# Performance work log

Hardware: AMD Instinct MI355X
Metric: run time of the kernel (lower is better)

## Reference

```python
import jax, jax.numpy as jnp
import numpy as np

INPUT_SIZE = 1024
HIDDEN_SIZE = 1024
BATCH = 4096


def setup_inputs() -> dict:
    key = jax.random.key(0)
    ks = jax.random.split(key, 20)
    k = 1.0 / HIDDEN_SIZE
    bound = float(np.sqrt(k))

    def u(kk, shape):
        return jax.random.uniform(kk, shape, jnp.float32, -bound, bound)

    inp = {
        "x": jax.random.normal(ks[0], (BATCH, INPUT_SIZE), jnp.float32),
        "h0": jax.random.normal(ks[1], (BATCH, HIDDEN_SIZE), jnp.float32),
        "c0": jax.random.normal(ks[2], (BATCH, HIDDEN_SIZE), jnp.float32),
        "W_ii": u(ks[3], (INPUT_SIZE, HIDDEN_SIZE)), "b_ii": u(ks[4], (HIDDEN_SIZE,)),
        "W_if": u(ks[5], (INPUT_SIZE, HIDDEN_SIZE)), "b_if": u(ks[6], (HIDDEN_SIZE,)),
        "W_ig": u(ks[7], (INPUT_SIZE, HIDDEN_SIZE)), "b_ig": u(ks[8], (HIDDEN_SIZE,)),
        "W_io": u(ks[9], (INPUT_SIZE, HIDDEN_SIZE)), "b_io": u(ks[10], (HIDDEN_SIZE,)),
        "W_hi": u(ks[11], (HIDDEN_SIZE, HIDDEN_SIZE)), "b_hi": u(ks[12], (HIDDEN_SIZE,)),
        "W_hf": u(ks[13], (HIDDEN_SIZE, HIDDEN_SIZE)), "b_hf": u(ks[14], (HIDDEN_SIZE,)),
        "W_hg": u(ks[15], (HIDDEN_SIZE, HIDDEN_SIZE)), "b_hg": u(ks[16], (HIDDEN_SIZE,)),
        "W_ho": u(ks[17], (HIDDEN_SIZE, HIDDEN_SIZE)), "b_ho": u(ks[18], (HIDDEN_SIZE,)),
    }
    return inp


def reference(x, h0, c0,
              W_ii, b_ii, W_if, b_if, W_ig, b_ig, W_io, b_io,
              W_hi, b_hi, W_hf, b_hf, W_hg, b_hg, W_ho, b_ho):
    # Fuse the 4 input-side and 4 hidden-side GEMMs into two wide GEMMs,
    # then a single fused gate computation — same math as the original.
    Wi = jnp.concatenate([W_ii, W_if, W_ig, W_io], axis=1)  # [In, 4H]
    Wh = jnp.concatenate([W_hi, W_hf, W_hg, W_ho], axis=1)  # [H, 4H]
    b = jnp.concatenate([b_ii + b_hi, b_if + b_hf, b_ig + b_hg, b_io + b_ho])
    gates = x @ Wi + h0 @ Wh + b  # [B, 4H]
    zi, zf, zg, zo = jnp.split(gates, 4, axis=1)
    i = jax.nn.sigmoid(zi)
    f = jax.nn.sigmoid(zf)
    g = jnp.tanh(zg)
    o = jax.nn.sigmoid(zo)
    c1 = f * c0 + i * g
    h1 = o * c1
    return h1, c1
```

## Files before the change

kernel.cpp:

```cpp
#include <hip/hip_runtime.h>

typedef unsigned short u16;
typedef unsigned int u32;
typedef __attribute__((ext_vector_type(8))) short short8;
typedef __attribute__((ext_vector_type(4))) float f32x4;

__device__ __forceinline__ u16 f2b(float f) {
  u32 u = __builtin_bit_cast(u32, f);
  u32 r = (u + 0x7FFFu + ((u >> 16) & 1u)) >> 16;
  return (u16)r;
}

__device__ __forceinline__ void gl_lds16(const void* g, void* l) {
  __builtin_amdgcn_global_load_lds(
      (const __attribute__((address_space(1))) u32*)g,
      (__attribute__((address_space(3))) u32*)l, 16, 0, 0);
}

struct Ptrs8 { const float* p[8]; };

__global__ __launch_bounds__(256) void wt_pack(Ptrs8 w, u16* __restrict__ Wt) {
  __shared__ float lds[64 * 64];
  const int tid = threadIdx.x;
  const int bid = blockIdx.x;
  const int mat = bid >> 8;
  const int g = mat & 3, h = mat >> 2;
  const int tile = bid & 255;
  const int kt = tile >> 4, nt = tile & 15;
  const float* __restrict__ src = w.p[mat];

#pragma unroll
  for (int i = 0; i < 4; ++i) {
    int c = tid + i * 256;
    int k = c >> 4, n4 = (c & 15) * 4;
    gl_lds16(src + (size_t)(kt * 64 + k) * 1024 + nt * 64 + n4, &lds[c * 4]);
  }
  asm volatile("s_waitcnt vmcnt(0)");
  __syncthreads();

#pragma unroll
  for (int i = 0; i < 2; ++i) {
    int c = tid + i * 256;
    int n = c & 63, kb = (c >> 6) * 8;
    short8 v;
#pragma unroll
    for (int j = 0; j < 8; ++j) v[j] = (short)f2b(lds[(kb + j) * 64 + n]);
    size_t off = (size_t)(g * 1024 + nt * 64 + n) * 2048 + h * 1024 + kt * 64 + kb;
    *reinterpret_cast<short8*>(Wt + off) = v;
  }
}

__global__ __launch_bounds__(256) void xh_pack(const float* __restrict__ x,
                                               const float* __restrict__ h0,
                                               u16* __restrict__ Ap) {
  int t = blockIdx.x * 256 + threadIdx.x;
  int m = t >> 8, kc = t & 255;
  const float* src = (kc < 128) ? (x + (size_t)m * 1024 + kc * 8)
                                : (h0 + (size_t)m * 1024 + (kc - 128) * 8);
  float4 a = *reinterpret_cast<const float4*>(src);
  float4 b = *reinterpret_cast<const float4*>(src + 4);
  short8 v;
  v[0] = (short)f2b(a.x); v[1] = (short)f2b(a.y);
  v[2] = (short)f2b(a.z); v[3] = (short)f2b(a.w);
  v[4] = (short)f2b(b.x); v[5] = (short)f2b(b.y);
  v[6] = (short)f2b(b.z); v[7] = (short)f2b(b.w);
  *reinterpret_cast<short8*>(Ap + (size_t)m * 2048 + kc * 8) = v;
}

__global__ void bias_pack(Ptrs8 b, float* __restrict__ bias) {
  int i = blockIdx.x * 1024 + threadIdx.x;
  int g = i >> 10, n = i & 1023;
  bias[i] = b.p[g][n] + b.p[4 + g][n];
}

#define LD8(base, off) (*reinterpret_cast<const short8*>((base) + (off)))
#define MFMA_(a, b, c) __builtin_amdgcn_mfma_f32_16x16x32_bf16(a, b, c, 0, 0, 0)
#define PIN asm volatile("" ::: "memory")
#define SB0 __builtin_amdgcn_sched_barrier(0)
#define BARR __builtin_amdgcn_s_barrier()
#define PRIO1 __builtin_amdgcn_s_setprio(1);
#define PRIO0 __builtin_amdgcn_s_setprio(0);

#define READ_A(DST, BASE)                                   \
  _Pragma("unroll")                                         \
  for (int mi = 0; mi < 4; ++mi) {                          \
    DST[mi][0] = LD8(Ab, arow + (BASE + mi) * 1024 + c0k);  \
    DST[mi][1] = LD8(Ab, arow + (BASE + mi) * 1024 + c1k);  \
  }
#define READ_B(DST, GB)                                     \
  _Pragma("unroll")                                         \
  for (int g = 0; g < 2; ++g) {                             \
    DST[g][0] = LD8(Bb, bbase + (GB + g) * 4096 + c0k);     \
    DST[g][1] = LD8(Bb, bbase + (GB + g) * 4096 + c1k);     \
  }
#define MFMA_QUAD(AF, BF, MO, GO)                                              \
  _Pragma("unroll")                                                            \
  for (int mi = 0; mi < 4; ++mi)                                               \
    _Pragma("unroll")                                                          \
    for (int g = 0; g < 2; ++g) {                                              \
      acc[MO + mi][GO + g] = MFMA_(AF[mi][0], BF[g][0], acc[MO + mi][GO + g]); \
      acc[MO + mi][GO + g] = MFMA_(AF[mi][1], BF[g][1], acc[MO + mi][GO + g]); \
    }

#define TILE4(BUF, T, ST, TAILW)                                             \
  {                                                                          \
    const u16* Ab = &As[BUF][0];                                             \
    const u16* Bb = &Bs[BUF][0];                                             \
    short8 af03[4][2], af47[4][2], bf01[2][2], bf23[2][2];                   \
                                               \
    READ_A(af03, 0) READ_B(bf01, 0) PIN;                                     \
    BARR;                                                                    \
    asm volatile("s_waitcnt lgkmcnt(0)"); SB0;                               \
    PRIO1 MFMA_QUAD(af03, bf01, 0, 0) PRIO0                                  \
    BARR; PIN;                                                               \
                                 \
    READ_B(bf23, 2) PIN;                                                     \
    if (ST) { stageA(BUF, (T) + 2, 0); stageB(BUF, (T) + 2, 0); }            \
    PIN;                                                                     \
    BARR;                                                                    \
    asm volatile("s_waitcnt lgkmcnt(0)"); SB0;                               \
    PRIO1 MFMA_QUAD(af03, bf23, 0, 2) PRIO0                                  \
    BARR; PIN;                                                               \
                                     \
    READ_A(af47, 4) PIN;                                                     \
    if (ST) { stageB(BUF, (T) + 2, 1); }                                     \
    PIN;                                                                     \
    BARR;                                                                    \
    asm volatile("s_waitcnt lgkmcnt(0)"); SB0;                               \
    PRIO1 MFMA_QUAD(af47, bf01, 4, 0) PRIO0                                  \
    BARR; PIN;                                                               \
                                       \
    if (ST) { stageA(BUF, (T) + 2, 1); }                                     \
    PIN;                                                                     \
    PRIO1 MFMA_QUAD(af47, bf23, 4, 2) PRIO0                                  \
    if ((TAILW) == 8) asm volatile("s_waitcnt vmcnt(8)" ::: "memory");       \
    else if ((TAILW) == 0) asm volatile("s_waitcnt vmcnt(0)" ::: "memory");  \
    BARR; PIN;                                                               \
  }

__global__ __launch_bounds__(512, 2) void lstm_fused(
    const u16* __restrict__ Ap, const float* __restrict__ c0,
    const u16* __restrict__ Wt, const float* __restrict__ bias,
    float* __restrict__ out) {
  __shared__ u16 As[2][256 * 64];
  __shared__ u16 Bs[2][256 * 64];

  const int tid = threadIdx.x;
  const int lane = tid & 63;
  const int wid = tid >> 6;
  const int wr = wid >> 2;
  const int wc = wid & 3;
  const int fl = lane & 15;
  const int hi = lane >> 4;
  const int lo7 = fl & 7;

  const int bid0 = blockIdx.x;
  const int sbid = (bid0 & 7) * 32 + (bid0 >> 3);
  const int m0 = (sbid >> 4) * 256;
  const int n0 = (sbid & 15) * 64;

  int aoff[4], boff[4];
#pragma unroll
  for (int i = 0; i < 4; ++i) {
    const int L = tid + i * 512;
    const int r = L >> 3, cL = L & 7;
    const int cg = cL ^ (r & 7);
    aoff[i] = (m0 + r) * 2048 + cg * 8;
    const int ge = r >> 6, wce = (r >> 4) & 3, ue = r & 15;
    boff[i] = (ge * 1024 + n0 + wce * 16 + ue) * 2048 + cg * 8;
  }

  auto stageA = [&](int buf, int t, int h) {
    const int k0 = t * 64;
    gl_lds16(Ap + aoff[h] + k0, &As[buf][(tid + h * 512) * 8]);
    gl_lds16(Ap + aoff[h + 2] + k0, &As[buf][(tid + (h + 2) * 512) * 8]);
  };
  auto stageB = [&](int buf, int t, int h) {
    const int k0 = t * 64;
    gl_lds16(Wt + boff[2 * h] + k0, &Bs[buf][(tid + (2 * h) * 512) * 8]);
    gl_lds16(Wt + boff[2 * h + 1] + k0, &Bs[buf][(tid + (2 * h + 1) * 512) * 8]);
  };

  const int c0k = (hi ^ lo7) * 8;
  const int c1k = ((4 + hi) ^ lo7) * 8;
  const int arow = (wr * 128 + fl) * 64;
  const int bbase = (wc * 16 + fl) * 64;

  f32x4 acc[8][4] = {};

  stageA(0, 0, 0); stageB(0, 0, 0); stageB(0, 0, 1); stageA(0, 0, 1);
  stageA(1, 1, 0); stageB(1, 1, 0); stageB(1, 1, 1); stageA(1, 1, 1);
  asm volatile("s_waitcnt vmcnt(8)" ::: "memory");
  BARR; PIN;

  for (int i = 0; i < 15; ++i) {
    TILE4(0, 2 * i, 1, 8)
    TILE4(1, 2 * i + 1, 1, 8)
  }
  TILE4(0, 30, 0, 0)
  TILE4(1, 31, 0, -1)

  const int col = n0 + wc * 16 + fl;
  float bv[4];
#pragma unroll
  for (int g = 0; g < 4; ++g) bv[g] = bias[g * 1024 + col];

#pragma unroll
  for (int mi = 0; mi < 8; ++mi) {
#pragma unroll
    for (int r = 0; r < 4; ++r) {
      const int row = m0 + wr * 128 + mi * 16 + hi * 4 + r;
      const float zi = acc[mi][0][r] + bv[0];
      const float zf = acc[mi][1][r] + bv[1];
      const float zg = acc[mi][2][r] + bv[2];
      const float zo = acc[mi][3][r] + bv[3];
      const float ig = 1.f / (1.f + __expf(-zi));
      const float fg = 1.f / (1.f + __expf(-zf));
      const float gg = 1.f - 2.f / (__expf(2.f * zg) + 1.f);
      const float og = 1.f / (1.f + __expf(-zo));
      const float c0v = c0[(size_t)row * 1024 + col];
      const float c1 = fg * c0v + ig * gg;
      const float h1 = og * c1;
      out[(size_t)row * 1024 + col] = h1;
      out[(size_t)4194304 + (size_t)row * 1024 + col] = c1;
    }
  }
}

extern "C" void kernel_launch(void* const* d_in, const int* in_sizes, int n_in,
                              void* d_out, int out_size, void* d_ws, size_t ws_size,
                              hipStream_t stream) {
  const float* x  = (const float*)d_in[0];
  const float* h0 = (const float*)d_in[1];
  const float* c0 = (const float*)d_in[2];
  Ptrs8 w, b;
  for (int i = 0; i < 4; ++i) {
    w.p[i]     = (const float*)d_in[3 + 2 * i];
    b.p[i]     = (const float*)d_in[4 + 2 * i];
    w.p[4 + i] = (const float*)d_in[11 + 2 * i];
    b.p[4 + i] = (const float*)d_in[12 + 2 * i];
  }
  u16* Wt = (u16*)d_ws;
  u16* Ap = (u16*)((char*)d_ws + (size_t)4096 * 2048 * 2);
  float* bias = (float*)((char*)d_ws + (size_t)2 * 4096 * 2048 * 2);
  float* out = (float*)d_out;

  wt_pack<<<2048, 256, 0, stream>>>(w, Wt);
  xh_pack<<<4096, 256, 0, stream>>>(x, h0, Ap);
  bias_pack<<<4, 1024, 0, stream>>>(b, bias);
  lstm_fused<<<256, 512, 0, stream>>>(Ap, c0, Wt, bias, out);
}
```

Measured before the change: 92.72 us.

## Merge pack kernels into one launch and restructure GEMM LDS pipeline

Merges the three preprocessing kernels (weight transpose and pack, activation pack, bias sum) into one prepack kernel that picks its role from the block index, which removes two launch gaps. The main LSTM GEMM loop now prefetches the next tile into the other buffer while computing the current one, instead of staging tile t+2 into the current buffer. It also trims the per-quarter barriers from two to one and uses finer vmcnt waits. The risk is a shorter prefetch distance, which may expose more global load latency, plus more delicate barrier and wait correctness.

```diff
diff --git a/kernel.cpp b/kernel.cpp
--- a/kernel.cpp
+++ b/kernel.cpp
@@ -19,67 +19,67 @@
 
 struct Ptrs8 { const float* p[8]; };
 
-__global__ __launch_bounds__(256) void wt_pack(Ptrs8 w, u16* __restrict__ Wt) {
+__global__ __launch_bounds__(256) void prepack(Ptrs8 w, Ptrs8 b,
+                                               const float* __restrict__ x,
+                                               const float* __restrict__ h0,
+                                               u16* __restrict__ Wt,
+                                               u16* __restrict__ Ap,
+                                               float* __restrict__ bias) {
   __shared__ float lds[64 * 64];
   const int tid = threadIdx.x;
   const int bid = blockIdx.x;
-  const int mat = bid >> 8;
-  const int g = mat & 3, h = mat >> 2;
-  const int tile = bid & 255;
-  const int kt = tile >> 4, nt = tile & 15;
-  const float* __restrict__ src = w.p[mat];
-
-#pragma unroll
-  for (int i = 0; i < 4; ++i) {
-    int c = tid + i * 256;
-    int k = c >> 4, n4 = (c & 15) * 4;
-    gl_lds16(src + (size_t)(kt * 64 + k) * 1024 + nt * 64 + n4, &lds[c * 4]);
-  }
-  asm volatile("s_waitcnt vmcnt(0)");
-  __syncthreads();
-
-#pragma unroll
-  for (int i = 0; i < 2; ++i) {
-    int c = tid + i * 256;
-    int n = c & 63, kb = (c >> 6) * 8;
+
+  if (bid < 2048) {
+    const int mat = bid >> 8;
+    const int g = mat & 3, h = mat >> 2;
+    const int tile = bid & 255;
+    const int kt = tile >> 4, nt = tile & 15;
+    const float* __restrict__ src = w.p[mat];
+#pragma unroll
+    for (int i = 0; i < 4; ++i) {
+      int c = tid + i * 256;
+      int k = c >> 4, n4 = (c & 15) * 4;
+      gl_lds16(src + (size_t)(kt * 64 + k) * 1024 + nt * 64 + n4, &lds[c * 4]);
+    }
+    asm volatile("s_waitcnt vmcnt(0)");
+    __syncthreads();
+#pragma unroll
+    for (int i = 0; i < 2; ++i) {
+      int c = tid + i * 256;
+      int n = c & 63, kb = (c >> 6) * 8;
+      short8 v;
+#pragma unroll
+      for (int j = 0; j < 8; ++j) v[j] = (short)f2b(lds[(kb + j) * 64 + n]);
+      size_t off = (size_t)(g * 1024 + nt * 64 + n) * 2048 + h * 1024 + kt * 64 + kb;
+      *reinterpret_cast<short8*>(Wt + off) = v;
+    }
+  } else if (bid < 6144) {
+    int t = (bid - 2048) * 256 + tid;
+    int m = t >> 8, kc = t & 255;
+    const float* src = (kc < 128) ? (x + (size_t)m * 1024 + kc * 8)
+                                  : (h0 + (size_t)m * 1024 + (kc - 128) * 8);
+    float4 a = *reinterpret_cast<const float4*>(src);
+    float4 bb = *reinterpret_cast<const float4*>(src + 4);
     short8 v;
-#pragma unroll
-    for (int j = 0; j < 8; ++j) v[j] = (short)f2b(lds[(kb + j) * 64 + n]);
-    size_t off = (size_t)(g * 1024 + nt * 64 + n) * 2048 + h * 1024 + kt * 64 + kb;
-    *reinterpret_cast<short8*>(Wt + off) = v;
-  }
-}
-
-__global__ __launch_bounds__(256) void xh_pack(const float* __restrict__ x,
-                                               const float* __restrict__ h0,
-                                               u16* __restrict__ Ap) {
-  int t = blockIdx.x * 256 + threadIdx.x;
-  int m = t >> 8, kc = t & 255;
-  const float* src = (kc < 128) ? (x + (size_t)m * 1024 + kc * 8)
-                                : (h0 + (size_t)m * 1024 + (kc - 128) * 8);
-  float4 a = *reinterpret_cast<const float4*>(src);
-  float4 b = *reinterpret_cast<const float4*>(src + 4);
-  short8 v;
-  v[0] = (short)f2b(a.x); v[1] = (short)f2b(a.y);
-  v[2] = (short)f2b(a.z); v[3] = (short)f2b(a.w);
-  v[4] = (short)f2b(b.x); v[5] = (short)f2b(b.y);
-  v[6] = (short)f2b(b.z); v[7] = (short)f2b(b.w);
-  *reinterpret_cast<short8*>(Ap + (size_t)m * 2048 + kc * 8) = v;
-}
-
-__global__ void bias_pack(Ptrs8 b, float* __restrict__ bias) {
-  int i = blockIdx.x * 1024 + threadIdx.x;
-  int g = i >> 10, n = i & 1023;
-  bias[i] = b.p[g][n] + b.p[4 + g][n];
+    v[0] = (short)f2b(a.x); v[1] = (short)f2b(a.y);
+    v[2] = (short)f2b(a.z); v[3] = (short)f2b(a.w);
+    v[4] = (short)f2b(bb.x); v[5] = (short)f2b(bb.y);
+    v[6] = (short)f2b(bb.z); v[7] = (short)f2b(bb.w);
+    *reinterpret_cast<short8*>(Ap + (size_t)m * 2048 + kc * 8) = v;
+  } else {
+    int i = (bid - 6144) * 256 + tid;
+    int g = i >> 10, n = i & 1023;
+    bias[i] = b.p[g][n] + b.p[4 + g][n];
+  }
 }
 
 #define LD8(base, off) (*reinterpret_cast<const short8*>((base) + (off)))
 #define MFMA_(a, b, c) __builtin_amdgcn_mfma_f32_16x16x32_bf16(a, b, c, 0, 0, 0)
-#define PIN asm volatile("" ::: "memory")
+#define BARR __builtin_amdgcn_s_barrier()
 #define SB0 __builtin_amdgcn_sched_barrier(0)
-#define BARR __builtin_amdgcn_s_barrier()
 #define PRIO1 __builtin_amdgcn_s_setprio(1);
 #define PRIO0 __builtin_amdgcn_s_setprio(0);
+#define PINM asm volatile("" ::: "memory")
 
 #define READ_A(DST, BASE)                                   \
   _Pragma("unroll")                                         \
@@ -102,40 +102,43 @@
       acc[MO + mi][GO + g] = MFMA_(AF[mi][1], BF[g][1], acc[MO + mi][GO + g]); \
     }
 
-#define TILE4(BUF, T, ST, TAILW)                                             \
+#define TILE4(CUR, T, ST, W1, W2, W4)                                        \
   {                                                                          \
-    const u16* Ab = &As[BUF][0];                                             \
-    const u16* Bb = &Bs[BUF][0];                                             \
+    const int nb = (CUR) ^ 1;                                                \
+    const u16* Ab = &As[CUR][0];                                             \
+    const u16* Bb = &Bs[CUR][0];                                             \
     short8 af03[4][2], af47[4][2], bf01[2][2], bf23[2][2];                   \
-                                               \
-    READ_A(af03, 0) READ_B(bf01, 0) PIN;                                     \
-    BARR;                                                                    \
+                             \
+    READ_A(af03, 0) READ_B(bf01, 0)                                          \
+    if (ST) stageA(nb, (T) + 1, 0);                                          \
     asm volatile("s_waitcnt lgkmcnt(0)"); SB0;                               \
     PRIO1 MFMA_QUAD(af03, bf01, 0, 0) PRIO0                                  \
-    BARR; PIN;                                                               \
-                                 \
-    READ_B(bf23, 2) PIN;                                                     \
-    if (ST) { stageA(BUF, (T) + 2, 0); stageB(BUF, (T) + 2, 0); }            \
-    PIN;                                                                     \
-    BARR;                                                                    \
+    if ((W1) == 4) asm volatile("s_waitcnt vmcnt(4)" ::: "memory");          \
+    else if ((W1) == 2) asm volatile("s_waitcnt vmcnt(2)" ::: "memory");     \
+    else PINM;                                                               \
+    BARR;                                                                    \
+                                          \
+    READ_A(af47, 4)                                                          \
+    if (ST) stageB(nb, (T) + 1, 0);                                          \
+    asm volatile("s_waitcnt lgkmcnt(0)"); SB0;                               \
+    PRIO1 MFMA_QUAD(af47, bf01, 4, 0) PRIO0                                  \
+    if ((W2) == 4) asm volatile("s_waitcnt vmcnt(4)" ::: "memory");          \
+    else if ((W2) == 0) asm volatile("s_waitcnt vmcnt(0)" ::: "memory");     \
+    else PINM;                                                               \
+    BARR;                                                                    \
+                                          \
+    READ_B(bf23, 2)                                                          \
+    if (ST) stageA(nb, (T) + 1, 1);                                          \
     asm volatile("s_waitcnt lgkmcnt(0)"); SB0;                               \
     PRIO1 MFMA_QUAD(af03, bf23, 0, 2) PRIO0                                  \
-    BARR; PIN;                                                               \
-                                     \
-    READ_A(af47, 4) PIN;                                                     \
-    if (ST) { stageB(BUF, (T) + 2, 1); }                                     \
-    PIN;                                                                     \
-    BARR;                                                                    \
-    asm volatile("s_waitcnt lgkmcnt(0)"); SB0;                               \
-    PRIO1 MFMA_QUAD(af47, bf01, 4, 0) PRIO0                                  \
-    BARR; PIN;                                                               \
-                                       \
-    if (ST) { stageA(BUF, (T) + 2, 1); }                                     \
-    PIN;                                                                     \
+    PINM;                                                                    \
+    BARR;                                                                    \
+                                           \
+    if (ST) stageB(nb, (T) + 1, 1);                                          \
     PRIO1 MFMA_QUAD(af47, bf23, 4, 2) PRIO0                                  \
-    if ((TAILW) == 8) asm volatile("s_waitcnt vmcnt(8)" ::: "memory");       \
-    else if ((TAILW) == 0) asm volatile("s_waitcnt vmcnt(0)" ::: "memory");  \
-    BARR; PIN;                                                               \
+    if ((W4) == 6) asm volatile("s_waitcnt vmcnt(6)" ::: "memory");          \
+    else PINM;                                                               \
+    BARR;                                                                    \
   }
 
 __global__ __launch_bounds__(512, 2) void lstm_fused(
@@ -188,17 +191,17 @@
 
   f32x4 acc[8][4] = {};
 
-  stageA(0, 0, 0); stageB(0, 0, 0); stageB(0, 0, 1); stageA(0, 0, 1);
-  stageA(1, 1, 0); stageB(1, 1, 0); stageB(1, 1, 1); stageA(1, 1, 1);
-  asm volatile("s_waitcnt vmcnt(8)" ::: "memory");
-  BARR; PIN;
-
-  for (int i = 0; i < 15; ++i) {
-    TILE4(0, 2 * i, 1, 8)
-    TILE4(1, 2 * i + 1, 1, 8)
-  }
-  TILE4(0, 30, 0, 0)
-  TILE4(1, 31, 0, -1)
+  stageA(0, 0, 0);
+  stageB(0, 0, 0);
+  stageA(0, 0, 1);
+  stageB(0, 0, 1);
+  asm volatile("s_waitcnt vmcnt(4)" ::: "memory");
+  BARR;
+
+  for (int t = 0; t < 31; ++t) {
+    TILE4(t & 1, t, 1, 4, 4, 6)
+  }
+  TILE4(1, 31, 0, 2, 0, -1)
 
   const int col = n0 + wc * 16 + fl;
   float bv[4];
@@ -245,8 +248,6 @@
   float* bias = (float*)((char*)d_ws + (size_t)2 * 4096 * 2048 * 2);
   float* out = (float*)d_out;
 
-  wt_pack<<<2048, 256, 0, stream>>>(w, Wt);
-  xh_pack<<<4096, 256, 0, stream>>>(x, h0, Ap);
-  bias_pack<<<4, 1024, 0, stream>>>(b, bias);
+  prepack<<<6160, 256, 0, stream>>>(w, b, x, h0, Wt, Ap, bias);
   lstm_fused<<<256, 512, 0, stream>>>(Ap, c0, Wt, bias, out);
 }
```

New measurement: 92.09 us. Within noise of the previous version (-0.7%).
